# Kernel optimization log

Hardware: AMD Instinct MI355X
Metric: run time of the kernel (lower is better)

The kernel has to match this reference:

```python
import jax, jax.numpy as jnp
import numpy as np

DEPTH, DIM, HEADS, DH = 2, 1024, 16, 64
B, N, MEM, TEXT = 8, 256, 4, 64
PH, PW, PS = 4, 4, 16
EXP_H, EXP_W, EXP_T = 4, 4, 2
RH, RW, RT = 2*EXP_H+1, 2*EXP_W+1, 2*EXP_T+1  # 9,9,5
CUR_IDX = 20
MEM_IDXS = [0, 5, 10, 15]
SCALE = DH ** -0.5


def _pos(idx):
    # get_pos_from_idx_down_right
    nf = PH * PW
    inner = idx % nf
    return inner % PH, inner // PH, idx // nf


def _axial_freqs():
    # 2D axial rotary freqs over the (PH*PS)x(PW*PS) pixel grid, rot_dim = DH
    GH, GW = PH * PS, PW * PS
    nfa = DH // 4  # 16 base freqs per axis -> 32 dims per axis after pair-repeat
    inv = 1.0 / (10000.0 ** (np.arange(nfa, dtype=np.float64) / nfa))
    fh = np.repeat(np.arange(GH)[:, None] * inv[None, :], 2, axis=-1)  # [GH,32]
    fw = np.repeat(np.arange(GW)[:, None] * inv[None, :], 2, axis=-1)  # [GW,32]
    return np.concatenate([
        np.broadcast_to(fh[:, None, :], (GH, GW, DH // 2)),
        np.broadcast_to(fw[None, :, :], (GH, GW, DH // 2)),
    ], axis=-1).astype(np.float32)  # [GH,GW,DH]


def setup_inputs() -> dict:
    key = jax.random.key(0)
    ks = jax.random.split(key, 14)
    p = lambda k, shape: jax.random.normal(k, shape, jnp.float32) * 0.02
    x = jax.random.normal(ks[0], (B, N, DIM), jnp.float32)
    cond = jax.random.normal(ks[1], (B, MEM * N + TEXT, DIM), jnp.float32)
    Wq = p(ks[2], (DEPTH, DIM, HEADS * DH))
    Wk = p(ks[3], (DEPTH, DIM, HEADS * DH))
    Wv = p(ks[4], (DEPTH, DIM, HEADS * DH))
    Wo = p(ks[5], (DEPTH, HEADS * DH, DIM))
    bo = jnp.zeros((DEPTH, DIM), jnp.float32)
    rpe = p(ks[6], (DEPTH, RH * RW * RT, HEADS))
    W1 = p(ks[7], (DEPTH, DIM, DIM * 4 * 2))
    b1 = jnp.zeros((DEPTH, DIM * 8), jnp.float32)
    W2 = p(ks[8], (DEPTH, DIM * 4, DIM))
    b2 = jnp.zeros((DEPTH, DIM), jnp.float32)
    freqs = _axial_freqs()
    def block(idx):
        r, c, _ = _pos(idx)
        return freqs[r * PS:(r + 1) * PS, c * PS:(c + 1) * PS].reshape(-1, DH)
    src_freq = jnp.asarray(block(CUR_IDX))
    tgt_freq = jnp.asarray(np.concatenate([block(i) for i in MEM_IDXS], axis=0))
    sr, sc, st = _pos(CUR_IDX)
    rel = [(tr - sr + EXP_H) * RW + (tc - sc + EXP_W) + (tt - st + EXP_T) * RH * RW
           for (tr, tc, tt) in map(_pos, MEM_IDXS)]
    rel_idx = jnp.asarray(rel, jnp.int32)
    return dict(x=x, cond=cond, Wq=Wq, Wk=Wk, Wv=Wv, Wo=Wo, bo=bo, rpe=rpe,
                W1=W1, b1=b1, W2=W2, b2=b2, src_freq=src_freq, tgt_freq=tgt_freq,
                rel_idx=rel_idx)


def _rotate_half(t):
    # pairs interleaved: (d r) with r=2
    tr = t.reshape(t.shape[:-1] + (-1, 2))
    t1, t2 = tr[..., 0], tr[..., 1]
    return jnp.stack((-t2, t1), axis=-1).reshape(t.shape)


def _apply_rotary(freqs, t):
    return t * jnp.cos(freqs) + _rotate_half(t) * jnp.sin(freqs)


def reference(x, cond, Wq, Wk, Wv, Wo, bo, rpe, W1, b1, W2, b2, src_freq, tgt_freq, rel_idx):
    MS = MEM * N  # memory token count in cond
    split_heads = lambda t: t.reshape(t.shape[0], t.shape[1], HEADS, DH).transpose(0, 2, 1, 3)
    for l in range(DEPTH):
        # --- FullCrossAttention ---
        q = split_heads(x @ Wq[l])          # [b,h,n,dh]
        k = split_heads(cond @ Wk[l])       # [b,h,j,dh]
        v = split_heads(cond @ Wv[l])
        # gathered relative-position bias added to k (broadcast over feature dim)
        bias = rpe[l][rel_idx]              # [mem, h]
        bias_k = jnp.repeat(bias.T, N, axis=1)[None, :, :, None]  # [1,h,mem*S,1]
        k = k.at[:, :, :MS, :].add(bias_k)
        # inline rotary: src freqs on q, gathered target freqs on memory keys
        q = _apply_rotary(src_freq, q)
        k = k.at[:, :, :MS, :].set(_apply_rotary(tgt_freq, k[:, :, :MS, :]))
        dots = jnp.einsum('bhid,bhjd->bhij', q, k) * SCALE
        attn = jax.nn.softmax(dots, axis=-1)
        out = jnp.einsum('bhij,bhjd->bhid', attn, v)
        out = out.transpose(0, 2, 1, 3).reshape(x.shape[0], N, HEADS * DH)
        x = x + out @ Wo[l] + bo[l]
        # --- GEGLU FeedForward ---
        hgl = x @ W1[l] + b1[l]
        a, g = jnp.split(hgl, 2, axis=-1)
        y = a * jax.nn.gelu(g, approximate=False)
        x = x + y @ W2[l] + b2[l]
    return x
```

## Files before the change

kernel.cpp:

```cpp
#include <hip/hip_runtime.h>
#include <hip/hip_bf16.h>
#include <math.h>

typedef __hip_bfloat16 bf16;
typedef __bf16 bf16x8 __attribute__((ext_vector_type(8)));
typedef float f32x4 __attribute__((ext_vector_type(4)));

typedef __attribute__((address_space(3))) void lds_void;
typedef const __attribute__((address_space(1))) void gbl_void;

__device__ __forceinline__ float b2f(bf16 v) { return __bfloat162float(v); }
__device__ __forceinline__ bf16 f2b(float v) { return __float2bfloat16(v); }

__device__ __forceinline__ f32x4 shfl_xor4(f32x4 v, int m) {
  f32x4 o;
  o[0] = __shfl_xor(v[0], m);
  o[1] = __shfl_xor(v[1], m);
  o[2] = __shfl_xor(v[2], m);
  o[3] = __shfl_xor(v[3], m);
  return o;
}
__device__ __forceinline__ f32x4 max4(f32x4 a, f32x4 b) {
  f32x4 o;
  o[0] = fmaxf(a[0], b[0]); o[1] = fmaxf(a[1], b[1]);
  o[2] = fmaxf(a[2], b[2]); o[3] = fmaxf(a[3], b[3]);
  return o;
}
__device__ __forceinline__ f32x4 exp4(f32x4 a) {
  f32x4 o;
  o[0] = __expf(a[0]); o[1] = __expf(a[1]);
  o[2] = __expf(a[2]); o[3] = __expf(a[3]);
  return o;
}

__global__ void detect_dtype(const unsigned int* __restrict__ x, int* __restrict__ flag) {
  int cnt = 0;
  for (int i = 0; i < 128; ++i) {
    unsigned int lo = x[i] & 0xFFFFu;
    unsigned int e = (lo >> 7) & 0xFFu;
    if (e >= 100u && e <= 140u) ++cnt;
  }
  *flag = (cnt >= 96) ? 1 : 0;
}

__global__ void convert_in(const void* __restrict__ src, bf16* __restrict__ dst,
                           int n, const int* __restrict__ flag) {
  int i = blockIdx.x * 256 + threadIdx.x;
  if (i >= n) return;
  dst[i] = (*flag) ? ((const bf16*)src)[i] : f2b(((const float*)src)[i]);
}

__global__ void emit_kernel(const float* __restrict__ xf, const int* __restrict__ flag,
                            void* __restrict__ out) {
  int i = blockIdx.x * 256 + threadIdx.x;
  if (*flag) ((bf16*)out)[i] = f2b(xf[i]);
  else       ((float*)out)[i] = xf[i];
}

template<int TAG>
__global__ __launch_bounds__(256, 2) void gemm_bt(
    const bf16* __restrict__ A, int lda,
    const bf16* __restrict__ Bt, int ldb,
    float alpha,
    const float* __restrict__ resid,
    const bf16* __restrict__ bias,
    float* __restrict__ outf,
    bf16* __restrict__ outb,
    int ldc, int K)
{
  __shared__ char smem[65536] __attribute__((aligned(16)));
  float* lC = (float*)smem;

  int tid = threadIdx.x;
  int lane = tid & 63;
  int wave = tid >> 6;
  int quad = lane >> 4, l16 = lane & 15;
  int wm = (wave >> 1) * 64, wn = (wave & 1) * 64;
  int row0 = blockIdx.y * 128, col0 = blockIdx.x * 128;

  const bf16* asrc[4]; const bf16* bsrc[4];
#pragma unroll
  for (int i = 0; i < 4; ++i) {
    int row = i * 32 + (tid >> 3);
    int coff = ((tid & 7) * 16) ^ ((row & 7) << 4);
    asrc[i] = A + (long long)(row0 + row) * lda + (coff >> 1);
    bsrc[i] = Bt + (long long)(col0 + row) * ldb + (coff >> 1);
  }
  int ldsbase = wave * 1024;

  f32x4 acc[4][4];
#pragma unroll
  for (int a = 0; a < 4; ++a)
#pragma unroll
    for (int b = 0; b < 4; ++b) acc[a][b] = (f32x4){0.f, 0.f, 0.f, 0.f};

  int nk = K >> 6;
#pragma unroll
  for (int i = 0; i < 4; ++i) {
    __builtin_amdgcn_global_load_lds((gbl_void*)(asrc[i]),
        (lds_void*)(smem + i * 4096 + ldsbase), 16, 0, 0);
    __builtin_amdgcn_global_load_lds((gbl_void*)(bsrc[i]),
        (lds_void*)(smem + 16384 + i * 4096 + ldsbase), 16, 0, 0);
  }
  __syncthreads();

  for (int t = 0; t < nk; ++t) {
    int buf = (t & 1) << 15;
    int nbuf = buf ^ 32768;
    if (t + 1 < nk) {
      int k0 = (t + 1) << 6;
#pragma unroll
      for (int i = 0; i < 4; ++i) {
        __builtin_amdgcn_global_load_lds((gbl_void*)(asrc[i] + k0),
            (lds_void*)(smem + nbuf + i * 4096 + ldsbase), 16, 0, 0);
        __builtin_amdgcn_global_load_lds((gbl_void*)(bsrc[i] + k0),
            (lds_void*)(smem + nbuf + 16384 + i * 4096 + ldsbase), 16, 0, 0);
      }
    }
    const __bf16* lA = (const __bf16*)(smem + buf);
    const __bf16* lB = (const __bf16*)(smem + buf + 16384);
#pragma unroll
    for (int ks = 0; ks < 2; ++ks) {
      bf16x8 af[4], bfr[4];
#pragma unroll
      for (int mi = 0; mi < 4; ++mi) {
        int r = wm + mi * 16 + l16;
        af[mi] = *(const bf16x8*)&lA[r * 64 + ((ks * 32 + quad * 8) ^ ((r & 7) << 3))];
      }
#pragma unroll
      for (int ni = 0; ni < 4; ++ni) {
        int r = wn + ni * 16 + l16;
        bfr[ni] = *(const bf16x8*)&lB[r * 64 + ((ks * 32 + quad * 8) ^ ((r & 7) << 3))];
      }
      __builtin_amdgcn_s_setprio(1);
#pragma unroll
      for (int mi = 0; mi < 4; ++mi)
#pragma unroll
        for (int ni = 0; ni < 4; ++ni)
          acc[mi][ni] = __builtin_amdgcn_mfma_f32_16x16x32_bf16(
              af[mi], bfr[ni], acc[mi][ni], 0, 0, 0);
      __builtin_amdgcn_s_setprio(0);
    }
    __syncthreads();
  }

#pragma unroll
  for (int half = 0; half < 2; ++half) {
    __syncthreads();
    if ((wave >> 1) == half) {
#pragma unroll
      for (int mi = 0; mi < 4; ++mi)
#pragma unroll
        for (int ni = 0; ni < 4; ++ni)
#pragma unroll
          for (int r = 0; r < 4; ++r)
            lC[(mi * 16 + quad * 4 + r) * 128 + wn + ni * 16 + l16] =
                acc[mi][ni][r] * alpha;
    }
    __syncthreads();
#pragma unroll
    for (int i = 0; i < 8; ++i) {
      int f = i * 256 + tid;
      int row = f >> 5, cc = (f & 31) * 4;
      int m = row0 + half * 64 + row, n = col0 + cc;
      f32x4 v = *(const f32x4*)&lC[row * 128 + cc];
      long long ci = (long long)m * ldc + n;
      if (bias) {
        v[0] += b2f(bias[n]);     v[1] += b2f(bias[n + 1]);
        v[2] += b2f(bias[n + 2]); v[3] += b2f(bias[n + 3]);
      }
      if (resid) v += *(const f32x4*)&resid[ci];
      if (outf) *(f32x4*)&outf[ci] = v;
      if (outb) {
        bf16 c0 = f2b(v[0]), c1 = f2b(v[1]), c2 = f2b(v[2]), c3 = f2b(v[3]);
        ushort4 o = { *(unsigned short*)&c0, *(unsigned short*)&c1,
                      *(unsigned short*)&c2, *(unsigned short*)&c3 };
        *(ushort4*)&outb[ci] = o;
      }
    }
  }
}

__global__ __launch_bounds__(512, 2) void gemm256(
    const bf16* __restrict__ A, int lda,
    const bf16* __restrict__ Bt, int ldb,
    const bf16* __restrict__ bias,
    bf16* __restrict__ outb,
    int ldc, int K)
{
  __shared__ char smem[131072] __attribute__((aligned(16)));
  float* lC = (float*)smem;

  int tid = threadIdx.x;
  int lane = tid & 63;
  int wave = tid >> 6;
  int quad = lane >> 4, l16 = lane & 15;
  int wr = wave >> 2, wc = wave & 3;
  int wm = wr * 128, wn = wc * 64;
  int row0 = blockIdx.y * 256, col0 = blockIdx.x * 256;

  const bf16* asrc[4]; const bf16* bsrc[4];
#pragma unroll
  for (int i = 0; i < 4; ++i) {
    int row = i * 64 + (tid >> 3);
    int coff = ((tid & 7) * 16) ^ ((row & 7) << 4);
    asrc[i] = A + (long long)(row0 + row) * lda + (coff >> 1);
    bsrc[i] = Bt + (long long)(col0 + row) * ldb + (coff >> 1);
  }
  int ldsbase = wave * 1024;

  f32x4 acc[8][4];
#pragma unroll
  for (int a = 0; a < 8; ++a)
#pragma unroll
    for (int b = 0; b < 4; ++b) acc[a][b] = (f32x4){0.f, 0.f, 0.f, 0.f};

  int nk = K >> 6;
#pragma unroll
  for (int i = 0; i < 4; ++i) {
    __builtin_amdgcn_global_load_lds((gbl_void*)(asrc[i]),
        (lds_void*)(smem + i * 8192 + ldsbase), 16, 0, 0);
    __builtin_amdgcn_global_load_lds((gbl_void*)(bsrc[i]),
        (lds_void*)(smem + 32768 + i * 8192 + ldsbase), 16, 0, 0);
  }
  __syncthreads();

  for (int t = 0; t < nk; ++t) {
    int buf = (t & 1) << 16;
    int nbuf = buf ^ 65536;
    if (t + 1 < nk) {
      int k0 = (t + 1) << 6;
#pragma unroll
      for (int i = 0; i < 4; ++i) {
        __builtin_amdgcn_global_load_lds((gbl_void*)(asrc[i] + k0),
            (lds_void*)(smem + nbuf + i * 8192 + ldsbase), 16, 0, 0);
        __builtin_amdgcn_global_load_lds((gbl_void*)(bsrc[i] + k0),
            (lds_void*)(smem + nbuf + 32768 + i * 8192 + ldsbase), 16, 0, 0);
      }
    }
    const __bf16* lA = (const __bf16*)(smem + buf);
    const __bf16* lB = (const __bf16*)(smem + buf + 32768);
#pragma unroll
    for (int ks = 0; ks < 2; ++ks) {
      bf16x8 af[8], bfr[4];
#pragma unroll
      for (int mi = 0; mi < 8; ++mi) {
        int r = wm + mi * 16 + l16;
        af[mi] = *(const bf16x8*)&lA[r * 64 + ((ks * 32 + quad * 8) ^ ((r & 7) << 3))];
      }
#pragma unroll
      for (int ni = 0; ni < 4; ++ni) {
        int r = wn + ni * 16 + l16;
        bfr[ni] = *(const bf16x8*)&lB[r * 64 + ((ks * 32 + quad * 8) ^ ((r & 7) << 3))];
      }
      __builtin_amdgcn_s_setprio(1);
#pragma unroll
      for (int mi = 0; mi < 8; ++mi)
#pragma unroll
        for (int ni = 0; ni < 4; ++ni)
          acc[mi][ni] = __builtin_amdgcn_mfma_f32_16x16x32_bf16(
              af[mi], bfr[ni], acc[mi][ni], 0, 0, 0);
      __builtin_amdgcn_s_setprio(0);
    }
    __syncthreads();
  }

#pragma unroll
  for (int h = 0; h < 2; ++h) {
    __syncthreads();
    if (wr == h) {
#pragma unroll
      for (int mi = 0; mi < 8; ++mi)
#pragma unroll
        for (int ni = 0; ni < 4; ++ni)
#pragma unroll
          for (int r = 0; r < 4; ++r)
            lC[(mi * 16 + quad * 4 + r) * 256 + wn + ni * 16 + l16] =
                acc[mi][ni][r];
    }
    __syncthreads();
#pragma unroll
    for (int it = 0; it < 16; ++it) {
      int f = it * 512 + tid;
      int row = f >> 6, cc = (f & 63) * 4;
      int m = row0 + h * 128 + row, n = col0 + cc;
      f32x4 v = *(const f32x4*)&lC[row * 256 + cc];
      v[0] += b2f(bias[n]);     v[1] += b2f(bias[n + 1]);
      v[2] += b2f(bias[n + 2]); v[3] += b2f(bias[n + 3]);
      bf16 c0 = f2b(v[0]), c1 = f2b(v[1]), c2 = f2b(v[2]), c3 = f2b(v[3]);
      ushort4 o = { *(unsigned short*)&c0, *(unsigned short*)&c1,
                    *(unsigned short*)&c2, *(unsigned short*)&c3 };
      *(ushort4*)&outb[(long long)m * ldc + n] = o;
    }
  }
}

__global__ __launch_bounds__(256, 2) void gemm_splitk(
    const bf16* __restrict__ A, int lda,
    const bf16* __restrict__ Bt, int ldb,
    float* __restrict__ pbuf, int ldc, int M, int KC)
{
  __shared__ char smem[65536] __attribute__((aligned(16)));

  int koff = blockIdx.z * KC;
  float* outz = pbuf + (long long)blockIdx.z * M * ldc;
  int tid = threadIdx.x;
  int lane = tid & 63;
  int wave = tid >> 6;
  int quad = lane >> 4, l16 = lane & 15;
  int wm = (wave >> 1) * 64, wn = (wave & 1) * 64;
  int row0 = blockIdx.y * 128, col0 = blockIdx.x * 128;

  const bf16* asrc[4]; const bf16* bsrc[4];
#pragma unroll
  for (int i = 0; i < 4; ++i) {
    int row = i * 32 + (tid >> 3);
    int coff = ((tid & 7) * 16) ^ ((row & 7) << 4);
    asrc[i] = A + (long long)(row0 + row) * lda + koff + (coff >> 1);
    bsrc[i] = Bt + (long long)(col0 + row) * ldb + koff + (coff >> 1);
  }
  int ldsbase = wave * 1024;

  f32x4 acc[4][4];
#pragma unroll
  for (int a = 0; a < 4; ++a)
#pragma unroll
    for (int b = 0; b < 4; ++b) acc[a][b] = (f32x4){0.f, 0.f, 0.f, 0.f};

  int nk = KC >> 6;
#pragma unroll
  for (int i = 0; i < 4; ++i) {
    __builtin_amdgcn_global_load_lds((gbl_void*)(asrc[i]),
        (lds_void*)(smem + i * 4096 + ldsbase), 16, 0, 0);
    __builtin_amdgcn_global_load_lds((gbl_void*)(bsrc[i]),
        (lds_void*)(smem + 16384 + i * 4096 + ldsbase), 16, 0, 0);
  }
  __syncthreads();

  for (int t = 0; t < nk; ++t) {
    int buf = (t & 1) << 15;
    int nbuf = buf ^ 32768;
    if (t + 1 < nk) {
      int k0 = (t + 1) << 6;
#pragma unroll
      for (int i = 0; i < 4; ++i) {
        __builtin_amdgcn_global_load_lds((gbl_void*)(asrc[i] + k0),
            (lds_void*)(smem + nbuf + i * 4096 + ldsbase), 16, 0, 0);
        __builtin_amdgcn_global_load_lds((gbl_void*)(bsrc[i] + k0),
            (lds_void*)(smem + nbuf + 16384 + i * 4096 + ldsbase), 16, 0, 0);
      }
    }
    const __bf16* lA = (const __bf16*)(smem + buf);
    const __bf16* lB = (const __bf16*)(smem + buf + 16384);
#pragma unroll
    for (int ks = 0; ks < 2; ++ks) {
      bf16x8 af[4], bfr[4];
#pragma unroll
      for (int mi = 0; mi < 4; ++mi) {
        int r = wm + mi * 16 + l16;
        af[mi] = *(const bf16x8*)&lA[r * 64 + ((ks * 32 + quad * 8) ^ ((r & 7) << 3))];
      }
#pragma unroll
      for (int ni = 0; ni < 4; ++ni) {
        int r = wn + ni * 16 + l16;
        bfr[ni] = *(const bf16x8*)&lB[r * 64 + ((ks * 32 + quad * 8) ^ ((r & 7) << 3))];
      }
      __builtin_amdgcn_s_setprio(1);
#pragma unroll
      for (int mi = 0; mi < 4; ++mi)
#pragma unroll
        for (int ni = 0; ni < 4; ++ni)
          acc[mi][ni] = __builtin_amdgcn_mfma_f32_16x16x32_bf16(
              af[mi], bfr[ni], acc[mi][ni], 0, 0, 0);
      __builtin_amdgcn_s_setprio(0);
    }
    __syncthreads();
  }

#pragma unroll
  for (int mi = 0; mi < 4; ++mi)
#pragma unroll
    for (int ni = 0; ni < 4; ++ni) {
      int n = col0 + wn + ni * 16 + l16;
#pragma unroll
      for (int r = 0; r < 4; ++r) {
        int m = row0 + wm + mi * 16 + quad * 4 + r;
        outz[(long long)m * ldc + n] = acc[mi][ni][r];
      }
    }
}

__global__ void reduce_ff2(const float* __restrict__ pbuf, const bf16* __restrict__ bias,
                           float* __restrict__ xf, bf16* __restrict__ xbf) {
  int i = blockIdx.x * 256 + threadIdx.x;
  const int NT = 2048 * 1024;
  float v = xf[i] + b2f(bias[i & 1023]) +
            pbuf[i] + pbuf[i + NT] + pbuf[i + 2 * NT] + pbuf[i + 3 * NT];
  xf[i] = v;
  xbf[i] = f2b(v);
}

__device__ __forceinline__ void fa_stage(
    const bf16* __restrict__ kb, const bf16* __restrict__ vtb, int j0, int tk,
    char* smem, int kboff, int vboff, int tid, int wave)
{
  int rounds = tk >> 6;
  for (int i = 0; i < rounds; ++i) {
    int rowk = i * 64 + (tid >> 3);
    int cbk = ((tid & 7) * 16) ^ ((rowk & 7) << 4);
    __builtin_amdgcn_global_load_lds(
        (gbl_void*)(kb + (long long)(j0 + rowk) * 1024 + (cbk >> 1)),
        (lds_void*)(smem + kboff + i * 8192 + wave * 1024), 16, 0, 0);
    int rowv, cbv;
    if (tk == 128) { rowv = i * 32 + (tid >> 4); cbv = ((tid & 15) * 16) ^ ((rowv & 7) << 4); }
    else           { rowv = (tid >> 3);          cbv = ((tid & 7) * 16) ^ ((rowv & 7) << 4); }
    __builtin_amdgcn_global_load_lds(
        (gbl_void*)(vtb + (long long)rowv * 8704 + j0 + (cbv >> 1)),
        (lds_void*)(smem + vboff + i * 8192 + wave * 1024), 16, 0, 0);
  }
}

template<int TK>
__device__ __forceinline__ void fa_compute(
    const char* smem, int kboff, int vboff,
    const bf16x8 (&qa)[2], bf16* lPw,
    int quad, int l16,
    f32x4 (&accO)[4], f32x4& mrow, f32x4& lrow)
{
  constexpr int NT = TK / 16;
  constexpr int NCH = TK / 32;
  const __bf16* lK = (const __bf16*)(smem + kboff);
  const __bf16* lV = (const __bf16*)(smem + vboff);
  int xork = (l16 & 7) << 3;

  f32x4 accS[NT];
#pragma unroll
  for (int ni = 0; ni < NT; ++ni) accS[ni] = (f32x4){0.f, 0.f, 0.f, 0.f};

#pragma unroll
  for (int ni = 0; ni < NT; ++ni)
#pragma unroll
    for (int ks = 0; ks < 2; ++ks) {
      bf16x8 bfr = *(const bf16x8*)&lK[(ni * 16 + l16) * 64 + ((ks * 32 + quad * 8) ^ xork)];
      accS[ni] = __builtin_amdgcn_mfma_f32_16x16x32_bf16(qa[ks], bfr, accS[ni], 0, 0, 0);
    }

  f32x4 vmax = (f32x4){-INFINITY, -INFINITY, -INFINITY, -INFINITY};
#pragma unroll
  for (int ni = 0; ni < NT; ++ni) {
    accS[ni] *= 0.125f;
    vmax = max4(vmax, accS[ni]);
  }
#pragma unroll
  for (int m = 1; m <= 8; m <<= 1) vmax = max4(vmax, shfl_xor4(vmax, m));
  f32x4 mnew = max4(mrow, vmax);
  f32x4 alpha = exp4(mrow - mnew);
  f32x4 rs = (f32x4){0.f, 0.f, 0.f, 0.f};
#pragma unroll
  for (int ni = 0; ni < NT; ++ni) {
    accS[ni] = exp4(accS[ni] - mnew);
    rs += accS[ni];
  }
#pragma unroll
  for (int m = 1; m <= 8; m <<= 1) rs += shfl_xor4(rs, m);
  lrow = lrow * alpha + rs;
  mrow = mnew;
#pragma unroll
  for (int nd = 0; nd < 4; ++nd) accO[nd] *= alpha;

#pragma unroll
  for (int c = 0; c < NCH; ++c) {
#pragma unroll
    for (int u = 0; u < 2; ++u)
#pragma unroll
      for (int r = 0; r < 4; ++r)
        lPw[(quad * 4 + r) * 40 + u * 16 + l16] = f2b(accS[c * 2 + u][r]);
    bf16x8 pa = *(const bf16x8*)&lPw[l16 * 40 + quad * 8];
#pragma unroll
    for (int nd = 0; nd < 4; ++nd) {
      bf16x8 vb = *(const bf16x8*)&lV[(nd * 16 + l16) * TK + ((c * 32 + quad * 8) ^ xork)];
      accO[nd] = __builtin_amdgcn_mfma_f32_16x16x32_bf16(pa, vb, accO[nd], 0, 0, 0);
    }
  }
}

__global__ __launch_bounds__(512, 2) void flash_attn(
    const bf16* __restrict__ q, const bf16* __restrict__ k,
    const bf16* __restrict__ vt, bf16* __restrict__ att)
{
  __shared__ char smem[75776] __attribute__((aligned(16)));

  int idx = blockIdx.x;
  int b = idx >> 5, h = (idx >> 1) & 15, half = idx & 1;
  int tid = threadIdx.x, wave = tid >> 6, lane = tid & 63;
  int quad = lane >> 4, l16 = lane & 15;
  int qrow0 = b * 256 + half * 128 + wave * 16;

  const bf16* kb  = k  + (long long)b * 1088 * 1024 + h * 64;
  const bf16* vtb = vt + (long long)(h * 64) * 8704 + b * 1088;
  bf16* lPw = (bf16*)(smem + 65536 + wave * 1280);

  bf16x8 qa[2];
#pragma unroll
  for (int ks = 0; ks < 2; ++ks)
    qa[ks] = *(const bf16x8*)&q[(long long)(qrow0 + l16) * 1024 +
                                h * 64 + ks * 32 + quad * 8];

  f32x4 accO[4];
  f32x4 mrow = (f32x4){-INFINITY, -INFINITY, -INFINITY, -INFINITY};
  f32x4 lrow = (f32x4){0.f, 0.f, 0.f, 0.f};
#pragma unroll
  for (int nd = 0; nd < 4; ++nd) accO[nd] = (f32x4){0.f, 0.f, 0.f, 0.f};

  fa_stage(kb, vtb, 0, 128, smem, 0, 32768, tid, wave);
  __syncthreads();

  for (int jt = 0; jt < 8; ++jt) {
    int buf = (jt & 1) * 16384;
    int nbuf = 16384 - buf;
    if (jt < 7) fa_stage(kb, vtb, (jt + 1) * 128, 128, smem, nbuf, 32768 + nbuf, tid, wave);
    else        fa_stage(kb, vtb, 1024, 64, smem, nbuf, 32768 + nbuf, tid, wave);
    fa_compute<128>(smem, buf, 32768 + buf, qa, lPw, quad, l16, accO, mrow, lrow);
    __syncthreads();
  }
  fa_compute<64>(smem, 0, 32768, qa, lPw, quad, l16, accO, mrow, lrow);

  f32x4 inv;
  inv[0] = 1.f / lrow[0]; inv[1] = 1.f / lrow[1];
  inv[2] = 1.f / lrow[2]; inv[3] = 1.f / lrow[3];
#pragma unroll
  for (int nd = 0; nd < 4; ++nd) {
    f32x4 o = accO[nd] * inv;
#pragma unroll
    for (int r = 0; r < 4; ++r)
      att[(long long)(qrow0 + quad * 4 + r) * 1024 +
          h * 64 + nd * 16 + l16] = f2b(o[r]);
  }
}

__global__ void init_x_kernel(const void* __restrict__ x, const int* __restrict__ flag,
                              float* __restrict__ xf, bf16* __restrict__ xbf) {
  int i = blockIdx.x * 256 + threadIdx.x;
  float v = (*flag) ? b2f(((const bf16*)x)[i]) : ((const float*)x)[i];
  xf[i] = v;
  xbf[i] = f2b(v);
}

__global__ void transpose_w(const void* __restrict__ in, bf16* __restrict__ out,
                            int R, int C, const int* __restrict__ flag) {
  __shared__ bf16 tile[32][33];
  long long zoff = (long long)blockIdx.z * R * C;
  const bf16* inb = (const bf16*)in + zoff;
  const float* inf = (const float*)in + zoff;
  out += zoff;
  int tx = threadIdx.x, ty = threadIdx.y;
  int c0 = blockIdx.x * 32, r0 = blockIdx.y * 32;
  int isb = *flag;
#pragma unroll
  for (int i = 0; i < 4; ++i) {
    long long off = (long long)(r0 + ty + i * 8) * C + (c0 + tx);
    tile[ty + i * 8][tx] = isb ? inb[off] : f2b(inf[off]);
  }
  __syncthreads();
#pragma unroll
  for (int i = 0; i < 4; ++i)
    out[(long long)(c0 + ty + i * 8) * R + (r0 + tx)] = tile[tx][ty + i * 8];
}

__global__ void rotary_q_kernel(bf16* __restrict__ q, const bf16* __restrict__ srcf) {
  int idx = blockIdx.x * 256 + threadIdx.x;
  int row = idx >> 9;
  int p = idx & 511;
  int h = p >> 5, i = p & 31;
  int d0 = h * 64 + 2 * i;
  int ntok = row & 255;
  float f = b2f(srcf[ntok * 64 + 2 * i]);
  float c = cosf(f), s = sinf(f);
  long long base = (long long)row * 1024 + d0;
  float q0 = b2f(q[base]), q1 = b2f(q[base + 1]);
  q[base]     = f2b(q0 * c - q1 * s);
  q[base + 1] = f2b(q1 * c + q0 * s);
}

__global__ void k_bias_rot_kernel(bf16* __restrict__ k, const bf16* __restrict__ tgtf,
                                  const bf16* __restrict__ rpe,
                                  const int* __restrict__ ridx, int layer) {
  int idx = blockIdx.x * 256 + threadIdx.x;
  int b = idx >> 19;
  int rem = idx & ((1 << 19) - 1);
  int j = rem >> 9;
  int p = rem & 511;
  int h = p >> 5, i = p & 31;
  int d0 = h * 64 + 2 * i;
  float bias = b2f(rpe[(layer * 405 + ridx[j >> 8]) * 16 + h]);
  float f = b2f(tgtf[j * 64 + 2 * i]);
  float c = cosf(f), s = sinf(f);
  long long base = (long long)(b * 1088 + j) * 1024 + d0;
  float k0 = b2f(k[base]) + bias, k1 = b2f(k[base + 1]) + bias;
  k[base]     = f2b(k0 * c - k1 * s);
  k[base + 1] = f2b(k1 * c + k0 * s);
}

__global__ void geglu_kernel(const bf16* __restrict__ hgl, bf16* __restrict__ y) {
  int idx = blockIdx.x * 256 + threadIdx.x;
  int m = idx >> 12, n = idx & 4095;
  float a = b2f(hgl[(long long)m * 8192 + n]);
  float g = b2f(hgl[(long long)m * 8192 + 4096 + n]);
  float ge = 0.5f * g * (1.0f + erff(g * 0.70710678118654752f));
  y[idx] = f2b(a * ge);
}

extern "C" void kernel_launch(void* const* d_in, const int* in_sizes, int n_in,
                              void* d_out, int out_size, void* d_ws, size_t ws_size,
                              hipStream_t stream) {
  (void)in_sizes; (void)n_in; (void)out_size; (void)ws_size;
  const void* x    = d_in[0];
  const void* cond = d_in[1];
  const void* Wq   = d_in[2];
  const void* Wk   = d_in[3];
  const void* Wv   = d_in[4];
  const void* Wo   = d_in[5];
  const void* bo   = d_in[6];
  const void* rpe  = d_in[7];
  const void* W1   = d_in[8];
  const void* b1   = d_in[9];
  const void* W2   = d_in[10];
  const void* b2   = d_in[11];
  const void* srcf = d_in[12];
  const void* tgtf = d_in[13];
  const int*  ridx = (const int*)d_in[14];

  char* w = (char*)d_ws;
  int* flag = (int*)w;   w += 256;
  bf16* WqT = (bf16*)w;  w += (size_t)2 * 1024 * 1024 * 2;
  bf16* WkT = (bf16*)w;  w += (size_t)2 * 1024 * 1024 * 2;
  bf16* WvT = (bf16*)w;  w += (size_t)2 * 1024 * 1024 * 2;
  bf16* WoT = (bf16*)w;  w += (size_t)2 * 1024 * 1024 * 2;
  bf16* W1T = (bf16*)w;  w += (size_t)2 * 8192 * 1024 * 2;
  bf16* W2T = (bf16*)w;  w += (size_t)2 * 4096 * 1024 * 2;
  bf16* condb = (bf16*)w; w += (size_t)8704 * 1024 * 2;
  bf16* bo_b = (bf16*)w;  w += 2048 * 2;
  bf16* rpe_b = (bf16*)w; w += 12960 * 2;
  bf16* b1_b = (bf16*)w;  w += 16384 * 2;
  bf16* b2_b = (bf16*)w;  w += 2048 * 2;
  bf16* srcf_b = (bf16*)w; w += 16384 * 2;
  bf16* tgtf_b = (bf16*)w; w += 65536 * 2;
  float* xf = (float*)w; w += (size_t)2048 * 1024 * 4;
  bf16* xbf = (bf16*)w;  w += (size_t)2048 * 1024 * 2;
  bf16* qbuf = (bf16*)w; w += (size_t)2048 * 1024 * 2;
  bf16* kbuf = (bf16*)w; w += (size_t)8704 * 1024 * 2;
  bf16* vTf = (bf16*)w;  w += (size_t)1024 * 8704 * 2;
  bf16* att = (bf16*)w;  w += (size_t)2048 * 1024 * 2;
  bf16* hgl = (bf16*)w;  w += (size_t)2048 * 8192 * 2;
  bf16* ybuf = (bf16*)w; w += (size_t)2048 * 4096 * 2;
  float* pbuf = (float*)hgl;

  detect_dtype<<<1, 1, 0, stream>>>((const unsigned int*)x, flag);

  convert_in<<<34816, 256, 0, stream>>>(cond, condb, 8704 * 1024, flag);
  convert_in<<<8, 256, 0, stream>>>(bo, bo_b, 2048, flag);
  convert_in<<<51, 256, 0, stream>>>(rpe, rpe_b, 12960, flag);
  convert_in<<<64, 256, 0, stream>>>(b1, b1_b, 16384, flag);
  convert_in<<<8, 256, 0, stream>>>(b2, b2_b, 2048, flag);
  convert_in<<<64, 256, 0, stream>>>(srcf, srcf_b, 16384, flag);
  convert_in<<<256, 256, 0, stream>>>(tgtf, tgtf_b, 65536, flag);

  dim3 tb(32, 8);
  transpose_w<<<dim3(32, 32, 2),  tb, 0, stream>>>(Wq, WqT, 1024, 1024, flag);
  transpose_w<<<dim3(32, 32, 2),  tb, 0, stream>>>(Wk, WkT, 1024, 1024, flag);
  transpose_w<<<dim3(32, 32, 2),  tb, 0, stream>>>(Wv, WvT, 1024, 1024, flag);
  transpose_w<<<dim3(32, 32, 2),  tb, 0, stream>>>(Wo, WoT, 1024, 1024, flag);
  transpose_w<<<dim3(256, 32, 2), tb, 0, stream>>>(W1, W1T, 1024, 8192, flag);
  transpose_w<<<dim3(32, 128, 2), tb, 0, stream>>>(W2, W2T, 4096, 1024, flag);
  init_x_kernel<<<8192, 256, 0, stream>>>(x, flag, xf, xbf);

  for (int l = 0; l < 2; ++l) {
    const bf16* WqTl = WqT + (size_t)l * 1024 * 1024;
    const bf16* WkTl = WkT + (size_t)l * 1024 * 1024;
    const bf16* WvTl = WvT + (size_t)l * 1024 * 1024;
    const bf16* WoTl = WoT + (size_t)l * 1024 * 1024;
    const bf16* W1Tl = W1T + (size_t)l * 8192 * 1024;
    const bf16* W2Tl = W2T + (size_t)l * 4096 * 1024;

    gemm_bt<0><<<dim3(8, 16), 256, 0, stream>>>(xbf, 1024, WqTl, 1024, 1.f,
        nullptr, nullptr, nullptr, qbuf, 1024, 1024);
    rotary_q_kernel<<<4096, 256, 0, stream>>>(qbuf, srcf_b);
    gemm_bt<1><<<dim3(68, 8), 256, 0, stream>>>(WvTl, 1024, condb, 1024, 1.f,
        nullptr, nullptr, nullptr, vTf, 8704, 1024);
    gemm_bt<2><<<dim3(8, 68), 256, 0, stream>>>(condb, 1024, WkTl, 1024, 1.f,
        nullptr, nullptr, nullptr, kbuf, 1024, 1024);
    k_bias_rot_kernel<<<16384, 256, 0, stream>>>(kbuf, tgtf_b, rpe_b, ridx, l);
    flash_attn<<<256, 512, 0, stream>>>(qbuf, kbuf, vTf, att);
    gemm_bt<3><<<dim3(8, 16), 256, 0, stream>>>(att, 1024, WoTl, 1024, 1.f,
        xf, bo_b + (size_t)l * 1024, xf, xbf, 1024, 1024);
    gemm256<<<dim3(32, 8), 512, 0, stream>>>(xbf, 1024, W1Tl, 1024,
        b1_b + (size_t)l * 8192, hgl, 8192, 1024);
    geglu_kernel<<<32768, 256, 0, stream>>>(hgl, ybuf);
    gemm_splitk<<<dim3(8, 16, 4), 256, 0, stream>>>(ybuf, 4096, W2Tl, 4096,
                                                    pbuf, 1024, 2048, 1024);
    reduce_ff2<<<8192, 256, 0, stream>>>(pbuf, b2_b + (size_t)l * 1024, xf, xbf);
  }

  emit_kernel<<<8192, 256, 0, stream>>>(xf, flag, d_out);
}
```

Baseline: 785.7 us.

## Use 4-stage BK=32 LDS ring with counted vmcnt waits in GEMMs

Changes all three GEMM kernels from a double-buffered BK=64 LDS pipeline to a four-slot ring of BK=32 tiles, prefetching three tiles ahead. The full __syncthreads is replaced by an explicit s_waitcnt vmcnt(N) plus s_barrier, so only the oldest in-flight tile has to land before compute. The LDS tile layout and swizzle change to pack two 64-row halves into each 64-byte-wide line. The aim is to hide global-load latency better. The cost is more barriers per unit of K and a fragile hand-coded vmcnt accounting that depends on the exact number of loads issued per stage.

```diff
diff --git a/kernel.cpp b/kernel.cpp
--- a/kernel.cpp
+++ b/kernel.cpp
@@ -33,6 +33,14 @@
   return o;
 }
 
+__device__ __forceinline__ void cbar(int ahead) {
+  if (ahead >= 2)      asm volatile("s_waitcnt vmcnt(8)" ::: "memory");
+  else if (ahead == 1) asm volatile("s_waitcnt vmcnt(4)" ::: "memory");
+  else                 asm volatile("s_waitcnt vmcnt(0)" ::: "memory");
+  __builtin_amdgcn_s_barrier();
+  __builtin_amdgcn_sched_barrier(0);
+}
+
 __global__ void detect_dtype(const unsigned int* __restrict__ x, int* __restrict__ flag) {
   int cnt = 0;
   for (int i = 0; i < 128; ++i) {
@@ -55,6 +63,14 @@
   int i = blockIdx.x * 256 + threadIdx.x;
   if (*flag) ((bf16*)out)[i] = f2b(xf[i]);
   else       ((float*)out)[i] = xf[i];
+}
+
+template<int HALF>
+__device__ __forceinline__ bf16x8 frag_ld(const __bf16* lt, int r, int quad) {
+  constexpr int LB = (HALF == 128) ? 7 : 6;
+  int line = r & (HALF - 1);
+  int sl = (((r >> LB) << 2) | quad) ^ (line & 7);
+  return *(const bf16x8*)&lt[line * 64 + sl * 8];
 }
 
 template<int TAG>
@@ -78,15 +94,27 @@
   int wm = (wave >> 1) * 64, wn = (wave & 1) * 64;
   int row0 = blockIdx.y * 128, col0 = blockIdx.x * 128;
 
-  const bf16* asrc[4]; const bf16* bsrc[4];
-#pragma unroll
-  for (int i = 0; i < 4; ++i) {
-    int row = i * 32 + (tid >> 3);
-    int coff = ((tid & 7) * 16) ^ ((row & 7) << 4);
-    asrc[i] = A + (long long)(row0 + row) * lda + (coff >> 1);
-    bsrc[i] = Bt + (long long)(col0 + row) * ldb + (coff >> 1);
-  }
-  int ldsbase = wave * 1024;
+  const bf16* asrc[2]; const bf16* bsrc[2];
+#pragma unroll
+  for (int i = 0; i < 2; ++i) {
+    int line = i * 32 + (tid >> 3);
+    int hx = (tid & 7) ^ (line & 7);
+    int r = line + ((hx >> 2) << 6);
+    int ke = (hx & 3) << 3;
+    asrc[i] = A + (long long)(row0 + r) * lda + ke;
+    bsrc[i] = Bt + (long long)(col0 + r) * ldb + ke;
+  }
+
+  auto stage = [&](int b, int t) {
+    int o = t * 32;
+#pragma unroll
+    for (int i = 0; i < 2; ++i) {
+      __builtin_amdgcn_global_load_lds((gbl_void*)(asrc[i] + o),
+          (lds_void*)(smem + b * 8192 + i * 4096 + wave * 1024), 16, 0, 0);
+      __builtin_amdgcn_global_load_lds((gbl_void*)(bsrc[i] + o),
+          (lds_void*)(smem + 32768 + b * 8192 + i * 4096 + wave * 1024), 16, 0, 0);
+    }
+  };
 
   f32x4 acc[4][4];
 #pragma unroll
@@ -94,54 +122,29 @@
 #pragma unroll
     for (int b = 0; b < 4; ++b) acc[a][b] = (f32x4){0.f, 0.f, 0.f, 0.f};
 
-  int nk = K >> 6;
-#pragma unroll
-  for (int i = 0; i < 4; ++i) {
-    __builtin_amdgcn_global_load_lds((gbl_void*)(asrc[i]),
-        (lds_void*)(smem + i * 4096 + ldsbase), 16, 0, 0);
-    __builtin_amdgcn_global_load_lds((gbl_void*)(bsrc[i]),
-        (lds_void*)(smem + 16384 + i * 4096 + ldsbase), 16, 0, 0);
-  }
-  __syncthreads();
+  int nk = K >> 5;
+  stage(0, 0); stage(1, 1); stage(2, 2);
+  cbar(2);
 
   for (int t = 0; t < nk; ++t) {
-    int buf = (t & 1) << 15;
-    int nbuf = buf ^ 32768;
-    if (t + 1 < nk) {
-      int k0 = (t + 1) << 6;
-#pragma unroll
-      for (int i = 0; i < 4; ++i) {
-        __builtin_amdgcn_global_load_lds((gbl_void*)(asrc[i] + k0),
-            (lds_void*)(smem + nbuf + i * 4096 + ldsbase), 16, 0, 0);
-        __builtin_amdgcn_global_load_lds((gbl_void*)(bsrc[i] + k0),
-            (lds_void*)(smem + nbuf + 16384 + i * 4096 + ldsbase), 16, 0, 0);
-      }
-    }
-    const __bf16* lA = (const __bf16*)(smem + buf);
-    const __bf16* lB = (const __bf16*)(smem + buf + 16384);
-#pragma unroll
-    for (int ks = 0; ks < 2; ++ks) {
-      bf16x8 af[4], bfr[4];
-#pragma unroll
-      for (int mi = 0; mi < 4; ++mi) {
-        int r = wm + mi * 16 + l16;
-        af[mi] = *(const bf16x8*)&lA[r * 64 + ((ks * 32 + quad * 8) ^ ((r & 7) << 3))];
-      }
-#pragma unroll
-      for (int ni = 0; ni < 4; ++ni) {
-        int r = wn + ni * 16 + l16;
-        bfr[ni] = *(const bf16x8*)&lB[r * 64 + ((ks * 32 + quad * 8) ^ ((r & 7) << 3))];
-      }
-      __builtin_amdgcn_s_setprio(1);
-#pragma unroll
-      for (int mi = 0; mi < 4; ++mi)
-#pragma unroll
-        for (int ni = 0; ni < 4; ++ni)
-          acc[mi][ni] = __builtin_amdgcn_mfma_f32_16x16x32_bf16(
-              af[mi], bfr[ni], acc[mi][ni], 0, 0, 0);
-      __builtin_amdgcn_s_setprio(0);
-    }
-    __syncthreads();
+    if (t + 3 < nk) stage((t + 3) & 3, t + 3);
+    const __bf16* lA = (const __bf16*)(smem + (t & 3) * 8192);
+    const __bf16* lB = (const __bf16*)(smem + 32768 + (t & 3) * 8192);
+    bf16x8 af[4], bfr[4];
+#pragma unroll
+    for (int mi = 0; mi < 4; ++mi) af[mi] = frag_ld<64>(lA, wm + mi * 16 + l16, quad);
+#pragma unroll
+    for (int ni = 0; ni < 4; ++ni) bfr[ni] = frag_ld<64>(lB, wn + ni * 16 + l16, quad);
+    __builtin_amdgcn_s_setprio(1);
+#pragma unroll
+    for (int mi = 0; mi < 4; ++mi)
+#pragma unroll
+      for (int ni = 0; ni < 4; ++ni)
+        acc[mi][ni] = __builtin_amdgcn_mfma_f32_16x16x32_bf16(
+            af[mi], bfr[ni], acc[mi][ni], 0, 0, 0);
+    __builtin_amdgcn_s_setprio(0);
+    int hi = t + 3; if (hi > nk - 1) hi = nk - 1;
+    cbar(hi - (t + 1));
   }
 
 #pragma unroll
@@ -199,15 +202,27 @@
   int wm = wr * 128, wn = wc * 64;
   int row0 = blockIdx.y * 256, col0 = blockIdx.x * 256;
 
-  const bf16* asrc[4]; const bf16* bsrc[4];
-#pragma unroll
-  for (int i = 0; i < 4; ++i) {
-    int row = i * 64 + (tid >> 3);
-    int coff = ((tid & 7) * 16) ^ ((row & 7) << 4);
-    asrc[i] = A + (long long)(row0 + row) * lda + (coff >> 1);
-    bsrc[i] = Bt + (long long)(col0 + row) * ldb + (coff >> 1);
-  }
-  int ldsbase = wave * 1024;
+  const bf16* asrc[2]; const bf16* bsrc[2];
+#pragma unroll
+  for (int i = 0; i < 2; ++i) {
+    int line = i * 64 + (tid >> 3);
+    int hx = (tid & 7) ^ (line & 7);
+    int r = line + ((hx >> 2) << 7);
+    int ke = (hx & 3) << 3;
+    asrc[i] = A + (long long)(row0 + r) * lda + ke;
+    bsrc[i] = Bt + (long long)(col0 + r) * ldb + ke;
+  }
+
+  auto stage = [&](int b, int t) {
+    int o = t * 32;
+#pragma unroll
+    for (int i = 0; i < 2; ++i) {
+      __builtin_amdgcn_global_load_lds((gbl_void*)(asrc[i] + o),
+          (lds_void*)(smem + b * 16384 + i * 8192 + wave * 1024), 16, 0, 0);
+      __builtin_amdgcn_global_load_lds((gbl_void*)(bsrc[i] + o),
+          (lds_void*)(smem + 65536 + b * 16384 + i * 8192 + wave * 1024), 16, 0, 0);
+    }
+  };
 
   f32x4 acc[8][4];
 #pragma unroll
@@ -215,54 +230,29 @@
 #pragma unroll
     for (int b = 0; b < 4; ++b) acc[a][b] = (f32x4){0.f, 0.f, 0.f, 0.f};
 
-  int nk = K >> 6;
-#pragma unroll
-  for (int i = 0; i < 4; ++i) {
-    __builtin_amdgcn_global_load_lds((gbl_void*)(asrc[i]),
-        (lds_void*)(smem + i * 8192 + ldsbase), 16, 0, 0);
-    __builtin_amdgcn_global_load_lds((gbl_void*)(bsrc[i]),
-        (lds_void*)(smem + 32768 + i * 8192 + ldsbase), 16, 0, 0);
-  }
-  __syncthreads();
+  int nk = K >> 5;
+  stage(0, 0); stage(1, 1); stage(2, 2);
+  cbar(2);
 
   for (int t = 0; t < nk; ++t) {
-    int buf = (t & 1) << 16;
-    int nbuf = buf ^ 65536;
-    if (t + 1 < nk) {
-      int k0 = (t + 1) << 6;
-#pragma unroll
-      for (int i = 0; i < 4; ++i) {
-        __builtin_amdgcn_global_load_lds((gbl_void*)(asrc[i] + k0),
-            (lds_void*)(smem + nbuf + i * 8192 + ldsbase), 16, 0, 0);
-        __builtin_amdgcn_global_load_lds((gbl_void*)(bsrc[i] + k0),
-            (lds_void*)(smem + nbuf + 32768 + i * 8192 + ldsbase), 16, 0, 0);
-      }
-    }
-    const __bf16* lA = (const __bf16*)(smem + buf);
-    const __bf16* lB = (const __bf16*)(smem + buf + 32768);
-#pragma unroll
-    for (int ks = 0; ks < 2; ++ks) {
-      bf16x8 af[8], bfr[4];
-#pragma unroll
-      for (int mi = 0; mi < 8; ++mi) {
-        int r = wm + mi * 16 + l16;
-        af[mi] = *(const bf16x8*)&lA[r * 64 + ((ks * 32 + quad * 8) ^ ((r & 7) << 3))];
-      }
-#pragma unroll
-      for (int ni = 0; ni < 4; ++ni) {
-        int r = wn + ni * 16 + l16;
-        bfr[ni] = *(const bf16x8*)&lB[r * 64 + ((ks * 32 + quad * 8) ^ ((r & 7) << 3))];
-      }
-      __builtin_amdgcn_s_setprio(1);
-#pragma unroll
-      for (int mi = 0; mi < 8; ++mi)
-#pragma unroll
-        for (int ni = 0; ni < 4; ++ni)
-          acc[mi][ni] = __builtin_amdgcn_mfma_f32_16x16x32_bf16(
-              af[mi], bfr[ni], acc[mi][ni], 0, 0, 0);
-      __builtin_amdgcn_s_setprio(0);
-    }
-    __syncthreads();
+    if (t + 3 < nk) stage((t + 3) & 3, t + 3);
+    const __bf16* lA = (const __bf16*)(smem + (t & 3) * 16384);
+    const __bf16* lB = (const __bf16*)(smem + 65536 + (t & 3) * 16384);
+    bf16x8 af[8], bfr[4];
+#pragma unroll
+    for (int mi = 0; mi < 8; ++mi) af[mi] = frag_ld<128>(lA, wm + mi * 16 + l16, quad);
+#pragma unroll
+    for (int ni = 0; ni < 4; ++ni) bfr[ni] = frag_ld<128>(lB, wn + ni * 16 + l16, quad);
+    __builtin_amdgcn_s_setprio(1);
+#pragma unroll
+    for (int mi = 0; mi < 8; ++mi)
+#pragma unroll
+      for (int ni = 0; ni < 4; ++ni)
+        acc[mi][ni] = __builtin_amdgcn_mfma_f32_16x16x32_bf16(
+            af[mi], bfr[ni], acc[mi][ni], 0, 0, 0);
+    __builtin_amdgcn_s_setprio(0);
+    int hi = t + 3; if (hi > nk - 1) hi = nk - 1;
+    cbar(hi - (t + 1));
   }
 
 #pragma unroll
@@ -311,15 +301,27 @@
   int wm = (wave >> 1) * 64, wn = (wave & 1) * 64;
   int row0 = blockIdx.y * 128, col0 = blockIdx.x * 128;
 
-  const bf16* asrc[4]; const bf16* bsrc[4];
-#pragma unroll
-  for (int i = 0; i < 4; ++i) {
-    int row = i * 32 + (tid >> 3);
-    int coff = ((tid & 7) * 16) ^ ((row & 7) << 4);
-    asrc[i] = A + (long long)(row0 + row) * lda + koff + (coff >> 1);
-    bsrc[i] = Bt + (long long)(col0 + row) * ldb + koff + (coff >> 1);
-  }
-  int ldsbase = wave * 1024;
+  const bf16* asrc[2]; const bf16* bsrc[2];
+#pragma unroll
+  for (int i = 0; i < 2; ++i) {
+    int line = i * 32 + (tid >> 3);
+    int hx = (tid & 7) ^ (line & 7);
+    int r = line + ((hx >> 2) << 6);
+    int ke = (hx & 3) << 3;
+    asrc[i] = A + (long long)(row0 + r) * lda + koff + ke;
+    bsrc[i] = Bt + (long long)(col0 + r) * ldb + koff + ke;
+  }
+
+  auto stage = [&](int b, int t) {
+    int o = t * 32;
+#pragma unroll
+    for (int i = 0; i < 2; ++i) {
+      __builtin_amdgcn_global_load_lds((gbl_void*)(asrc[i] + o),
+          (lds_void*)(smem + b * 8192 + i * 4096 + wave * 1024), 16, 0, 0);
+      __builtin_amdgcn_global_load_lds((gbl_void*)(bsrc[i] + o),
+          (lds_void*)(smem + 32768 + b * 8192 + i * 4096 + wave * 1024), 16, 0, 0);
+    }
+  };
 
   f32x4 acc[4][4];
 #pragma unroll
@@ -327,54 +329,29 @@
 #pragma unroll
     for (int b = 0; b < 4; ++b) acc[a][b] = (f32x4){0.f, 0.f, 0.f, 0.f};
 
-  int nk = KC >> 6;
-#pragma unroll
-  for (int i = 0; i < 4; ++i) {
-    __builtin_amdgcn_global_load_lds((gbl_void*)(asrc[i]),
-        (lds_void*)(smem + i * 4096 + ldsbase), 16, 0, 0);
-    __builtin_amdgcn_global_load_lds((gbl_void*)(bsrc[i]),
-        (lds_void*)(smem + 16384 + i * 4096 + ldsbase), 16, 0, 0);
-  }
-  __syncthreads();
+  int nk = KC >> 5;
+  stage(0, 0); stage(1, 1); stage(2, 2);
+  cbar(2);
 
   for (int t = 0; t < nk; ++t) {
-    int buf = (t & 1) << 15;
-    int nbuf = buf ^ 32768;
-    if (t + 1 < nk) {
-      int k0 = (t + 1) << 6;
-#pragma unroll
-      for (int i = 0; i < 4; ++i) {
-        __builtin_amdgcn_global_load_lds((gbl_void*)(asrc[i] + k0),
-            (lds_void*)(smem + nbuf + i * 4096 + ldsbase), 16, 0, 0);
-        __builtin_amdgcn_global_load_lds((gbl_void*)(bsrc[i] + k0),
-            (lds_void*)(smem + nbuf + 16384 + i * 4096 + ldsbase), 16, 0, 0);
-      }
-    }
-    const __bf16* lA = (const __bf16*)(smem + buf);
-    const __bf16* lB = (const __bf16*)(smem + buf + 16384);
-#pragma unroll
-    for (int ks = 0; ks < 2; ++ks) {
-      bf16x8 af[4], bfr[4];
-#pragma unroll
-      for (int mi = 0; mi < 4; ++mi) {
-        int r = wm + mi * 16 + l16;
-        af[mi] = *(const bf16x8*)&lA[r * 64 + ((ks * 32 + quad * 8) ^ ((r & 7) << 3))];
-      }
-#pragma unroll
-      for (int ni = 0; ni < 4; ++ni) {
-        int r = wn + ni * 16 + l16;
-        bfr[ni] = *(const bf16x8*)&lB[r * 64 + ((ks * 32 + quad * 8) ^ ((r & 7) << 3))];
-      }
-      __builtin_amdgcn_s_setprio(1);
-#pragma unroll
-      for (int mi = 0; mi < 4; ++mi)
-#pragma unroll
-        for (int ni = 0; ni < 4; ++ni)
-          acc[mi][ni] = __builtin_amdgcn_mfma_f32_16x16x32_bf16(
-              af[mi], bfr[ni], acc[mi][ni], 0, 0, 0);
-      __builtin_amdgcn_s_setprio(0);
-    }
-    __syncthreads();
+    if (t + 3 < nk) stage((t + 3) & 3, t + 3);
+    const __bf16* lA = (const __bf16*)(smem + (t & 3) * 8192);
+    const __bf16* lB = (const __bf16*)(smem + 32768 + (t & 3) * 8192);
+    bf16x8 af[4], bfr[4];
+#pragma unroll
+    for (int mi = 0; mi < 4; ++mi) af[mi] = frag_ld<64>(lA, wm + mi * 16 + l16, quad);
+#pragma unroll
+    for (int ni = 0; ni < 4; ++ni) bfr[ni] = frag_ld<64>(lB, wn + ni * 16 + l16, quad);
+    __builtin_amdgcn_s_setprio(1);
+#pragma unroll
+    for (int mi = 0; mi < 4; ++mi)
+#pragma unroll
+      for (int ni = 0; ni < 4; ++ni)
+        acc[mi][ni] = __builtin_amdgcn_mfma_f32_16x16x32_bf16(
+            af[mi], bfr[ni], acc[mi][ni], 0, 0, 0);
+    __builtin_amdgcn_s_setprio(0);
+    int hi = t + 3; if (hi > nk - 1) hi = nk - 1;
+    cbar(hi - (t + 1));
   }
 
 #pragma unroll
```

Result: no change. 783.9 us (-0.2%).
